# Kernel optimization log

Hardware: AMD Instinct MI355X
Metric: run time of the kernel (lower is better)

## Reference

```python
import jax, jax.numpy as jnp
import numpy as np

DIM = 64
D = DIM // 2
COND_DIM = 64
HIDDEN = 512
N_BINS = 8
TAIL = 3.0
MIN_BW = 1e-3
MIN_BH = 1e-3
MIN_DER = 1e-3
MAX_DER = 10.0
EPS = 1e-6
BATCH = 131072


def _pad_left_zero(x):
    # pad last axis with one leading zero
    pads = [(0, 0)] * (x.ndim - 1) + [(1, 0)]
    return jnp.pad(x, pads)


def rq_spline_forward(inputs, widths, heights, derivatives):
    # inputs: [B, D2]; widths/heights: [B, D2, K]; derivatives: [B, D2, K+1]
    num_bins = widths.shape[-1]
    left, right = -TAIL, TAIL
    bottom, top = -TAIL, TAIL

    w = jax.nn.softmax(widths, axis=-1) * (right - left - MIN_BW * num_bins) + MIN_BW
    cumw = _pad_left_zero(jnp.cumsum(w, axis=-1)) + left          # [B, D2, K+1]
    w = cumw[..., 1:] - cumw[..., :-1]

    h = jax.nn.softmax(heights, axis=-1) * (top - bottom - MIN_BH * num_bins) + MIN_BH
    cumh = _pad_left_zero(jnp.cumsum(h, axis=-1)) + bottom        # [B, D2, K+1]
    h = cumh[..., 1:] - cumh[..., :-1]

    der = jnp.minimum(jax.nn.softplus(derivatives) + MIN_DER, MAX_DER)  # [B, D2, K+1]

    inside = (inputs >= left) & (inputs <= right)
    x = jnp.clip(inputs, left, right)

    # data-dependent bin search
    bin_idx = jnp.sum((x[..., None] >= cumw[..., 1:]).astype(jnp.int32), axis=-1)
    bin_idx = jnp.clip(bin_idx, 0, num_bins - 1)

    def gth(t):
        return jnp.take_along_axis(t, bin_idx[..., None], axis=-1)[..., 0]

    in_cumw = gth(cumw[..., :-1] if False else cumw)  # cumwidths gather uses same idx
    in_cumw = gth(cumw)
    in_bw = jnp.maximum(gth(w), EPS)
    out_cumh = gth(cumh)
    out_bh = gth(h)
    delta = out_bh / in_bw
    d_left = gth(der[..., :-1])
    d_right = gth(der[..., 1:])

    theta = (x - in_cumw) / in_bw
    tomt = theta * (1.0 - theta)
    numer = out_bh * (delta * theta**2 + d_left * tomt)
    denom = jnp.maximum(delta + (d_left + d_right - 2.0 * delta) * tomt, EPS)
    out_inside = out_cumh + numer / denom

    der_num = delta**2 * (d_right * theta**2 + 2.0 * delta * tomt + d_left * (1.0 - theta) ** 2)
    der_den = denom**2
    der_num = jnp.maximum(der_num, EPS)
    der_den = jnp.maximum(der_den, EPS)
    lad_inside = jnp.log(der_num) - jnp.log(der_den) - jnp.log(in_bw)

    outputs = jnp.where(inside, out_inside, inputs)
    logabsdet = jnp.where(inside, lad_inside, 0.0)

    outputs = jnp.nan_to_num(outputs, nan=0.0, posinf=TAIL, neginf=-TAIL)
    logabsdet = jnp.nan_to_num(logabsdet, nan=0.0, posinf=0.0, neginf=0.0)
    return outputs, logabsdet


def setup_inputs() -> dict:
    key = jax.random.key(0)
    ks = jax.random.split(key, 8)
    in_dim = D + COND_DIM
    out_dim = (DIM - D) * (3 * N_BINS + 1)
    s1 = 1.0 / np.sqrt(in_dim)
    s2 = 1.0 / np.sqrt(HIDDEN)
    return {
        "z": jax.random.normal(ks[0], (BATCH, DIM), jnp.float32),
        "condition": jax.random.normal(ks[1], (BATCH, COND_DIM), jnp.float32),
        "W1": jax.random.normal(ks[2], (in_dim, HIDDEN), jnp.float32) * s1,
        "b1": jnp.zeros((HIDDEN,), jnp.float32),
        "W2": jax.random.normal(ks[3], (HIDDEN, HIDDEN), jnp.float32) * s2,
        "b2": jnp.zeros((HIDDEN,), jnp.float32),
        "W3": jax.random.normal(ks[4], (HIDDEN, out_dim), jnp.float32) * s2,
        "b3": jnp.zeros((out_dim,), jnp.float32),
    }


def reference(z, condition, W1, b1, W2, b2, W3, b3):
    z1, z2 = z[:, :D], z[:, D:]
    x = jnp.concatenate([z1, condition], axis=1)
    hdd = jax.nn.relu(x @ W1 + b1)
    hdd = jax.nn.relu(hdd @ W2 + b2)
    params = hdd @ W3 + b3                                   # [B, (DIM-D)*(3K+1)]
    params = params.reshape(params.shape[0], DIM - D, 3 * N_BINS + 1)
    widths = params[..., :N_BINS]
    heights = params[..., N_BINS:2 * N_BINS]
    derivs = params[..., 2 * N_BINS:]
    z2_new, logabsdet = rq_spline_forward(z2, widths, heights, derivs)
    log_det = jnp.sum(logabsdet, axis=1)
    return jnp.concatenate([z1, z2_new], axis=1), log_det
```

## Files before the change

### kernel.cpp

```cpp
#include <hip/hip_runtime.h>
#include <hip/hip_fp16.h>


typedef _Float16 f16x8 __attribute__((ext_vector_type(8)));
typedef float f32x4 __attribute__((ext_vector_type(4)));

#define MROWS 32
#define XS 104
#define NWAVES 8
#define TPB 512

#define OFF_H1 0
#define OFF_L1 49152
#define OFF_H2 98304
#define OFF_L2 360448
#define OFF_H3 622592
#define OFF_L3 1032192
#define WS_HALVES 1441792

#define SMEM_BYTES 144384

__global__ __launch_bounds__(256) void prep_weights(
    const float* __restrict__ W1, const float* __restrict__ W2,
    const float* __restrict__ W3, _Float16* __restrict__ ws)
{
  int idx = blockIdx.x * 256 + threadIdx.x;
  float v; int hoff, loff;
  if (idx < 49152) {
    int n = idx / 96, k = idx - n * 96;
    v = W1[k * 512 + n];
    hoff = OFF_H1 + idx; loff = OFF_L1 + idx;
  } else if (idx < 311296) {
    int i = idx - 49152;
    int n = i >> 9, k = i & 511;
    v = W2[k * 512 + n];
    hoff = OFF_H2 + i; loff = OFF_L2 + i;
  } else if (idx < 720896) {
    int i = idx - 311296;
    int n = i >> 9, k = i & 511;
    v = W3[k * 800 + n];
    hoff = OFF_H3 + i; loff = OFF_L3 + i;
  } else {
    return;
  }
  _Float16 hi = (_Float16)v;
  _Float16 lo = (_Float16)(v - (float)hi);
  ws[hoff] = hi; ws[loff] = lo;
}

__device__ __forceinline__ void mfma3(f32x4& c, f16x8 aH, f16x8 aL, f16x8 bH, f16x8 bL) {
  c = __builtin_amdgcn_mfma_f32_16x16x32_f16(aH, bH, c, 0, 0, 0);
  c = __builtin_amdgcn_mfma_f32_16x16x32_f16(aL, bH, c, 0, 0, 0);
  c = __builtin_amdgcn_mfma_f32_16x16x32_f16(aH, bL, c, 0, 0, 0);
}

__device__ __forceinline__ int swz(int row, int col) {
  return row * 512 + ((((col >> 3) ^ (row & 7)) << 3) | (col & 7));
}

__global__ __launch_bounds__(TPB, 2) void fused_flow(
    const float* __restrict__ z, const float* __restrict__ cond,
    const float* __restrict__ b1, const float* __restrict__ b2,
    const float* __restrict__ b3, const _Float16* __restrict__ ws,
    float* __restrict__ out, int B)
{
  extern __shared__ char smem[];
  _Float16* h1H = (_Float16*)(smem);
  _Float16* h1L = (_Float16*)(smem + 32768);
  _Float16* h2H = (_Float16*)(smem + 65536);
  _Float16* h2L = (_Float16*)(smem + 98304);
  _Float16* xH  = (_Float16*)(smem + 131072);
  _Float16* xL  = (_Float16*)(smem + 137728);
  float* pbuf   = (float*)(smem);

  const int tid  = threadIdx.x;
  const int lane = tid & 63;
  const int wave = tid >> 6;
  const int r15  = lane & 15;
  const int g4   = lane >> 4;
  const int row0 = blockIdx.x * MROWS;

  const _Float16* w1H = ws + OFF_H1; const _Float16* w1L = ws + OFF_L1;
  const _Float16* w2H = ws + OFF_H2; const _Float16* w2L = ws + OFF_L2;
  const _Float16* w3H = ws + OFF_H3; const _Float16* w3L = ws + OFF_L3;

  #pragma unroll
  for (int rep = 0; rep < 2; ++rep) {
    int i = tid + rep * TPB;
    int r = i >> 5, c = i & 31;
    out[(row0 + r) * 64 + c] = z[(row0 + r) * 64 + c];
  }

  #pragma unroll
  for (int rep = 0; rep < 6; ++rep) {
    int i = tid + rep * TPB;
    int r = i / 96, c = i - r * 96;
    float v = (c < 32) ? z[(row0 + r) * 64 + c] : cond[(row0 + r) * 64 + (c - 32)];
    _Float16 hi = (_Float16)v;
    xH[r * XS + c] = hi;
    xL[r * XS + c] = (_Float16)(v - (float)hi);
  }
  __syncthreads();

  f32x4 acc[2][4];
  #pragma unroll
  for (int mt = 0; mt < 2; ++mt)
    #pragma unroll
    for (int t = 0; t < 4; ++t)
      acc[mt][t] = (f32x4){0.f, 0.f, 0.f, 0.f};

  #pragma unroll
  for (int ks = 0; ks < 3; ++ks) {
    int kb = ks * 32 + g4 * 8;
    f16x8 a0H = *(const f16x8*)(xH + r15 * XS + kb);
    f16x8 a0L = *(const f16x8*)(xL + r15 * XS + kb);
    f16x8 a1H = *(const f16x8*)(xH + (r15 + 16) * XS + kb);
    f16x8 a1L = *(const f16x8*)(xL + (r15 + 16) * XS + kb);
    #pragma unroll
    for (int t = 0; t < 4; ++t) {
      int ncol = (wave * 4 + t) * 16 + r15;
      f16x8 bH = *(const f16x8*)(w1H + ncol * 96 + kb);
      f16x8 bL = *(const f16x8*)(w1L + ncol * 96 + kb);
      mfma3(acc[0][t], a0H, a0L, bH, bL);
      mfma3(acc[1][t], a1H, a1L, bH, bL);
    }
  }
  #pragma unroll
  for (int t = 0; t < 4; ++t) {
    int ncol = (wave * 4 + t) * 16 + r15;
    float bias = b1[ncol];
    #pragma unroll
    for (int mt = 0; mt < 2; ++mt)
      #pragma unroll
      for (int i = 0; i < 4; ++i) {
        int row = mt * 16 + g4 * 4 + i;
        float v = fmaxf(acc[mt][t][i] + bias, 0.f);
        _Float16 hi = (_Float16)v;
        int off = swz(row, ncol);
        h1H[off] = hi;
        h1L[off] = (_Float16)(v - (float)hi);
      }
  }
  __syncthreads();

  #pragma unroll
  for (int mt = 0; mt < 2; ++mt)
    #pragma unroll
    for (int t = 0; t < 4; ++t)
      acc[mt][t] = (f32x4){0.f, 0.f, 0.f, 0.f};

  for (int ks = 0; ks < 16; ++ks) {
    int kb = ks * 32 + g4 * 8;
    int g = kb >> 3;
    int o0 = r15 * 512 + (((g ^ (r15 & 7)) << 3));
    int o1 = (r15 + 16) * 512 + (((g ^ (r15 & 7)) << 3));
    f16x8 a0H = *(const f16x8*)(h1H + o0);
    f16x8 a0L = *(const f16x8*)(h1L + o0);
    f16x8 a1H = *(const f16x8*)(h1H + o1);
    f16x8 a1L = *(const f16x8*)(h1L + o1);
    #pragma unroll
    for (int t = 0; t < 4; ++t) {
      int ncol = (wave * 4 + t) * 16 + r15;
      f16x8 bH = *(const f16x8*)(w2H + ncol * 512 + kb);
      f16x8 bL = *(const f16x8*)(w2L + ncol * 512 + kb);
      mfma3(acc[0][t], a0H, a0L, bH, bL);
      mfma3(acc[1][t], a1H, a1L, bH, bL);
    }
  }
  #pragma unroll
  for (int t = 0; t < 4; ++t) {
    int ncol = (wave * 4 + t) * 16 + r15;
    float bias = b2[ncol];
    #pragma unroll
    for (int mt = 0; mt < 2; ++mt)
      #pragma unroll
      for (int i = 0; i < 4; ++i) {
        int row = mt * 16 + g4 * 4 + i;
        float v = fmaxf(acc[mt][t][i] + bias, 0.f);
        _Float16 hi = (_Float16)v;
        int off = swz(row, ncol);
        h2H[off] = hi;
        h2L[off] = (_Float16)(v - (float)hi);
      }
  }
  __syncthreads();

  f32x4 acc3[2][7];
  #pragma unroll
  for (int mt = 0; mt < 2; ++mt)
    #pragma unroll
    for (int tt = 0; tt < 7; ++tt)
      acc3[mt][tt] = (f32x4){0.f, 0.f, 0.f, 0.f};

  for (int ks = 0; ks < 16; ++ks) {
    int kb = ks * 32 + g4 * 8;
    int g = kb >> 3;
    int o0 = r15 * 512 + (((g ^ (r15 & 7)) << 3));
    int o1 = (r15 + 16) * 512 + (((g ^ (r15 & 7)) << 3));
    f16x8 a0H = *(const f16x8*)(h2H + o0);
    f16x8 a0L = *(const f16x8*)(h2L + o0);
    f16x8 a1H = *(const f16x8*)(h2H + o1);
    f16x8 a1L = *(const f16x8*)(h2L + o1);
    #pragma unroll
    for (int tt = 0; tt < 7; ++tt) {
      int nt = wave + tt * 8;
      if (nt < 50) {
        int ncol = nt * 16 + r15;
        f16x8 bH = *(const f16x8*)(w3H + ncol * 512 + kb);
        f16x8 bL = *(const f16x8*)(w3L + ncol * 512 + kb);
        mfma3(acc3[0][tt], a0H, a0L, bH, bL);
        mfma3(acc3[1][tt], a1H, a1L, bH, bL);
      }
    }
  }

  float logdet_part = 0.f;
  const int sr  = tid >> 4;
  const int sdl = tid & 15;

  #pragma unroll 1
  for (int c = 0; c < 2; ++c) {
    __syncthreads();
    #pragma unroll
    for (int tt = 0; tt < 7; ++tt) {
      int nt = wave + tt * 8;
      if (nt >= c * 25 && nt < c * 25 + 25) {
        int ncolg = nt * 16 + r15;
        int ncoll = ncolg - c * 400;
        float bias = b3[ncolg];
        #pragma unroll
        for (int mt = 0; mt < 2; ++mt)
          #pragma unroll
          for (int i = 0; i < 4; ++i) {
            int row = mt * 16 + g4 * 4 + i;
            pbuf[row * 401 + ncoll] = acc3[mt][tt][i] + bias;
          }
      }
    }
    __syncthreads();

    {
      int dim = c * 16 + sdl;
      float p[25];
      #pragma unroll
      for (int j = 0; j < 25; ++j) p[j] = pbuf[sr * 401 + sdl * 25 + j];

      float cw[9], ch[9], dv[9];
      {
        float m = p[0];
        #pragma unroll
        for (int j = 1; j < 8; ++j) m = fmaxf(m, p[j]);
        float e[8]; float s = 0.f;
        #pragma unroll
        for (int j = 0; j < 8; ++j) { e[j] = __expf(p[j] - m); s += e[j]; }
        float inv = 5.992f / s;
        cw[0] = -3.f; float a = 0.f;
        #pragma unroll
        for (int j = 0; j < 8; ++j) { a += e[j] * inv + 0.001f; cw[j + 1] = a - 3.f; }
      }
      {
        float m = p[8];
        #pragma unroll
        for (int j = 1; j < 8; ++j) m = fmaxf(m, p[8 + j]);
        float e[8]; float s = 0.f;
        #pragma unroll
        for (int j = 0; j < 8; ++j) { e[j] = __expf(p[8 + j] - m); s += e[j]; }
        float inv = 5.992f / s;
        ch[0] = -3.f; float a = 0.f;
        #pragma unroll
        for (int j = 0; j < 8; ++j) { a += e[j] * inv + 0.001f; ch[j + 1] = a - 3.f; }
      }
      #pragma unroll
      for (int j = 0; j < 9; ++j) {
        float t = p[16 + j];
        float sp = fmaxf(t, 0.f) + log1pf(__expf(-fabsf(t)));
        dv[j] = fminf(sp + 0.001f, 10.f);
      }

      float xin = z[(row0 + sr) * 64 + 32 + dim];
      bool inside = (xin >= -3.f) && (xin <= 3.f);
      float xc = fminf(fmaxf(xin, -3.f), 3.f);
      int b = 0;
      #pragma unroll
      for (int j = 1; j <= 8; ++j) b += (xc >= cw[j]) ? 1 : 0;
      if (b > 7) b = 7;

      float icw = cw[0], icw1 = cw[1], och = ch[0], och1 = ch[1], dl0 = dv[0], dr0 = dv[1];
      #pragma unroll
      for (int j = 1; j < 8; ++j) {
        bool sel = (b == j);
        icw  = sel ? cw[j]     : icw;
        icw1 = sel ? cw[j + 1] : icw1;
        och  = sel ? ch[j]     : och;
        och1 = sel ? ch[j + 1] : och1;
        dl0  = sel ? dv[j]     : dl0;
        dr0  = sel ? dv[j + 1] : dr0;
      }
      float ibw   = fmaxf(icw1 - icw, 1e-6f);
      float obh   = och1 - och;
      float delta = obh / ibw;
      float th    = (xc - icw) / ibw;
      float om    = 1.f - th;
      float tomt  = th * om;
      float numer = obh * (delta * th * th + dl0 * tomt);
      float denom = fmaxf(delta + (dl0 + dr0 - 2.f * delta) * tomt, 1e-6f);
      float outi  = och + numer / denom;
      float dn    = delta * delta * (dr0 * th * th + 2.f * delta * tomt + dl0 * om * om);
      float dd    = denom * denom;
      dn = fmaxf(dn, 1e-6f); dd = fmaxf(dd, 1e-6f);
      float lad   = __logf(dn) - __logf(dd) - __logf(ibw);

      float outv = inside ? outi : xin;
      float ladv = inside ? lad : 0.f;

      out[(row0 + sr) * 64 + 32 + dim] = outv;

      float s = ladv;
      s += __shfl_xor(s, 1);
      s += __shfl_xor(s, 2);
      s += __shfl_xor(s, 4);
      s += __shfl_xor(s, 8);
      if (sdl == 0) logdet_part += s;
    }
  }
  if (sdl == 0) out[(size_t)B * 64 + row0 + sr] = logdet_part;
}

extern "C" void kernel_launch(void* const* d_in, const int* in_sizes, int n_in,
                              void* d_out, int out_size, void* d_ws, size_t ws_size,
                              hipStream_t stream) {
  const float* z    = (const float*)d_in[0];
  const float* cnd  = (const float*)d_in[1];
  const float* W1   = (const float*)d_in[2];
  const float* b1   = (const float*)d_in[3];
  const float* W2   = (const float*)d_in[4];
  const float* b2   = (const float*)d_in[5];
  const float* W3   = (const float*)d_in[6];
  const float* b3   = (const float*)d_in[7];
  float* out        = (float*)d_out;
  _Float16* ws      = (_Float16*)d_ws;

  int B = in_sizes[0] / 64;

  hipFuncSetAttribute((const void*)fused_flow,
                      hipFuncAttributeMaxDynamicSharedMemorySize, SMEM_BYTES);

  prep_weights<<<(720896 + 255) / 256, 256, 0, stream>>>(W1, W2, W3, ws);
  fused_flow<<<B / MROWS, TPB, SMEM_BYTES, stream>>>(z, cnd, b1, b2, b3, ws, out, B);
}
```

Before: 1.553 ms.

## Reuse one hidden-activation LDS buffer across layers to raise occupancy

Layers one and two now share a single hi/lo fp16 activation buffer in shared memory instead of using separate h1 and h2 buffers, which cuts the shared-memory footprint from about 141 KB to 77 KB. An extra barrier is added so all waves finish reading layer-1 activations before layer-2 results overwrite them. Launch bounds are raised from 2 to 4 blocks per multiprocessor so more workgroups can be resident to hide weight-load latency. The tighter launch bound lowers the per-thread register budget and may cause spills in the wide accumulator arrays.

```diff
diff --git a/kernel.cpp b/kernel.cpp
--- a/kernel.cpp
+++ b/kernel.cpp
@@ -7,7 +7,6 @@
 
 #define MROWS 32
 #define XS 104
-#define NWAVES 8
 #define TPB 512
 
 #define OFF_H1 0
@@ -16,9 +15,8 @@
 #define OFF_L2 360448
 #define OFF_H3 622592
 #define OFF_L3 1032192
-#define WS_HALVES 1441792
-
-#define SMEM_BYTES 144384
+
+#define SMEM_BYTES 78848
 
 __global__ __launch_bounds__(256) void prep_weights(
     const float* __restrict__ W1, const float* __restrict__ W2,
@@ -58,19 +56,17 @@
   return row * 512 + ((((col >> 3) ^ (row & 7)) << 3) | (col & 7));
 }
 
-__global__ __launch_bounds__(TPB, 2) void fused_flow(
+__global__ __launch_bounds__(TPB, 4) void fused_flow(
     const float* __restrict__ z, const float* __restrict__ cond,
     const float* __restrict__ b1, const float* __restrict__ b2,
     const float* __restrict__ b3, const _Float16* __restrict__ ws,
     float* __restrict__ out, int B)
 {
   extern __shared__ char smem[];
-  _Float16* h1H = (_Float16*)(smem);
-  _Float16* h1L = (_Float16*)(smem + 32768);
-  _Float16* h2H = (_Float16*)(smem + 65536);
-  _Float16* h2L = (_Float16*)(smem + 98304);
-  _Float16* xH  = (_Float16*)(smem + 131072);
-  _Float16* xL  = (_Float16*)(smem + 137728);
+  _Float16* hbH = (_Float16*)(smem);
+  _Float16* hbL = (_Float16*)(smem + 32768);
+  _Float16* xH  = (_Float16*)(smem + 65536);
+  _Float16* xL  = (_Float16*)(smem + 72192);
   float* pbuf   = (float*)(smem);
 
   const int tid  = threadIdx.x;
@@ -137,8 +133,8 @@
         float v = fmaxf(acc[mt][t][i] + bias, 0.f);
         _Float16 hi = (_Float16)v;
         int off = swz(row, ncol);
-        h1H[off] = hi;
-        h1L[off] = (_Float16)(v - (float)hi);
+        hbH[off] = hi;
+        hbL[off] = (_Float16)(v - (float)hi);
       }
   }
   __syncthreads();
@@ -154,10 +150,10 @@
     int g = kb >> 3;
     int o0 = r15 * 512 + (((g ^ (r15 & 7)) << 3));
     int o1 = (r15 + 16) * 512 + (((g ^ (r15 & 7)) << 3));
-    f16x8 a0H = *(const f16x8*)(h1H + o0);
-    f16x8 a0L = *(const f16x8*)(h1L + o0);
-    f16x8 a1H = *(const f16x8*)(h1H + o1);
-    f16x8 a1L = *(const f16x8*)(h1L + o1);
+    f16x8 a0H = *(const f16x8*)(hbH + o0);
+    f16x8 a0L = *(const f16x8*)(hbL + o0);
+    f16x8 a1H = *(const f16x8*)(hbH + o1);
+    f16x8 a1L = *(const f16x8*)(hbL + o1);
     #pragma unroll
     for (int t = 0; t < 4; ++t) {
       int ncol = (wave * 4 + t) * 16 + r15;
@@ -167,6 +163,7 @@
       mfma3(acc[1][t], a1H, a1L, bH, bL);
     }
   }
+  __syncthreads();
   #pragma unroll
   for (int t = 0; t < 4; ++t) {
     int ncol = (wave * 4 + t) * 16 + r15;
@@ -179,8 +176,8 @@
         float v = fmaxf(acc[mt][t][i] + bias, 0.f);
         _Float16 hi = (_Float16)v;
         int off = swz(row, ncol);
-        h2H[off] = hi;
-        h2L[off] = (_Float16)(v - (float)hi);
+        hbH[off] = hi;
+        hbL[off] = (_Float16)(v - (float)hi);
       }
   }
   __syncthreads();
@@ -197,10 +194,10 @@
     int g = kb >> 3;
     int o0 = r15 * 512 + (((g ^ (r15 & 7)) << 3));
     int o1 = (r15 + 16) * 512 + (((g ^ (r15 & 7)) << 3));
-    f16x8 a0H = *(const f16x8*)(h2H + o0);
-    f16x8 a0L = *(const f16x8*)(h2L + o0);
-    f16x8 a1H = *(const f16x8*)(h2H + o1);
-    f16x8 a1L = *(const f16x8*)(h2L + o1);
+    f16x8 a0H = *(const f16x8*)(hbH + o0);
+    f16x8 a0L = *(const f16x8*)(hbL + o0);
+    f16x8 a1H = *(const f16x8*)(hbH + o1);
+    f16x8 a1L = *(const f16x8*)(hbL + o1);
     #pragma unroll
     for (int tt = 0; tt < 7; ++tt) {
       int nt = wave + tt * 8;
```

Result: faster. 1.464 ms (-5.7%).
